# Kernel tuning notes

Measured on AMD Instinct MI355X. Metric: run time of the kernel, lower is better.

Reference implementation:

```python
import jax, jax.numpy as jnp
import numpy as np
from jax import lax


def _maxpool_h(x):
    # MaxPool2d(kernel=(3,1), stride=(2,1), padding=(1,0)) on NCHW.
    # Torch pads with -inf for max pooling.
    return lax.reduce_window(
        x,
        -jnp.inf,
        lax.max,
        window_dimensions=(1, 1, 3, 1),
        window_strides=(1, 1, 2, 1),
        padding=((0, 0), (0, 0), (1, 1), (0, 0)),
    )


def setup_inputs() -> dict:
    key = jax.random.key(0)
    x = jax.random.normal(key, (32, 1, 8192, 256), dtype=jnp.float32)
    return {"x": x}


def reference(x) -> jnp.ndarray:
    out = _maxpool_h(x)  # [B, C, H', W]
    # Per-sample min-max normalization (vectorized over batch instead of the
    # original per-sample python loop).
    mx = jnp.max(out, axis=(1, 2, 3), keepdims=True)
    mn = jnp.min(out, axis=(1, 2, 3), keepdims=True)
    return (out - mn) / (mx - mn)
```

## Files before the change

kernel.cpp:

```cpp
#include <hip/hip_runtime.h>
#include <cfloat>

#define BATCH     32
#define H_IN      8192
#define H_OUT     4096
#define W         256
#define W4        64
#define CH        32
#define BLK_PER_B 32

__device__ __forceinline__ float4 max3_f4(float4 a, float4 b, float4 c) {
    float4 m;
    m.x = fmaxf(a.x, fmaxf(b.x, c.x));
    m.y = fmaxf(a.y, fmaxf(b.y, c.y));
    m.z = fmaxf(a.z, fmaxf(b.z, c.z));
    m.w = fmaxf(a.w, fmaxf(b.w, c.w));
    return m;
}

__global__ __launch_bounds__(256) void pool_partial(
        const float* __restrict__ x, float* __restrict__ out,
        float* __restrict__ partial_min, float* __restrict__ partial_max) {
    const int batch = blockIdx.x >> 5;
    const int blk   = blockIdx.x & 31;
    const int tid   = threadIdx.x;
    const int w4    = tid & 63;
    const int rg    = tid >> 6;
    const int h0    = blk * (BLK_PER_B * 4) + rg * CH;

    const float4* xin = (const float4*)x + (size_t)batch * H_IN * W4 + w4;
    float4*       po  = (float4*)out + ((size_t)batch * H_OUT + h0) * W4 + w4;

    float lmin = FLT_MAX, lmax = -FLT_MAX;

    float4 prev;
    const int r0 = 2 * h0 - 1;
    if (r0 >= 0) prev = xin[(size_t)r0 * W4];
    else         prev = make_float4(-FLT_MAX, -FLT_MAX, -FLT_MAX, -FLT_MAX);

    #pragma unroll 4
    for (int i = 0; i < CH; ++i) {
        const int r = 2 * (h0 + i);
        float4 a = xin[(size_t)r * W4];
        float4 c = xin[(size_t)(r + 1) * W4];
        float4 m = max3_f4(prev, a, c);
        po[(size_t)i * W4] = m;
        prev = c;
        lmax = fmaxf(lmax, fmaxf(fmaxf(m.x, m.y), fmaxf(m.z, m.w)));
        lmin = fminf(lmin, fminf(fminf(m.x, m.y), fminf(m.z, m.w)));
    }

    #pragma unroll
    for (int off = 32; off > 0; off >>= 1) {
        lmax = fmaxf(lmax, __shfl_down(lmax, off, 64));
        lmin = fminf(lmin, __shfl_down(lmin, off, 64));
    }
    __shared__ float smax[4], smin[4];
    const int lane = tid & 63;
    if (lane == 0) { smax[rg] = lmax; smin[rg] = lmin; }
    __syncthreads();
    if (tid == 0) {
        float bmax = smax[0], bmin = smin[0];
        #pragma unroll
        for (int i = 1; i < 4; ++i) {
            bmax = fmaxf(bmax, smax[i]);
            bmin = fminf(bmin, smin[i]);
        }
        partial_max[blockIdx.x] = bmax;
        partial_min[blockIdx.x] = bmin;
    }
}

__global__ void reduce_partials(const float* __restrict__ pmin,
                                const float* __restrict__ pmax,
                                float* __restrict__ stats) {
    const int b = blockIdx.x;
    const int t = threadIdx.x;
    float mn = (t < BLK_PER_B) ? pmin[b * BLK_PER_B + t] : FLT_MAX;
    float mx = (t < BLK_PER_B) ? pmax[b * BLK_PER_B + t] : -FLT_MAX;
    #pragma unroll
    for (int off = 16; off > 0; off >>= 1) {
        mn = fminf(mn, __shfl_down(mn, off, 64));
        mx = fmaxf(mx, __shfl_down(mx, off, 64));
    }
    if (t == 0) {
        stats[2 * b]     = mn;
        stats[2 * b + 1] = 1.0f / (mx - mn);
    }
}

__global__ __launch_bounds__(256) void normalize(float* __restrict__ out,
                                                 const float* __restrict__ stats) {
    const int b   = blockIdx.x >> 8;
    const int blk = blockIdx.x & 255;
    const float mn  = stats[2 * b];
    const float inv = stats[2 * b + 1];
    float4* p = (float4*)out + (size_t)b * (H_OUT * W4);
    const int base = blk * 1024 + threadIdx.x;
    #pragma unroll
    for (int i = 0; i < 4; ++i) {
        const int idx = base + i * 256;
        float4 v = p[idx];
        v.x = (v.x - mn) * inv;
        v.y = (v.y - mn) * inv;
        v.z = (v.z - mn) * inv;
        v.w = (v.w - mn) * inv;
        p[idx] = v;
    }
}

extern "C" void kernel_launch(void* const* d_in, const int* in_sizes, int n_in,
                              void* d_out, int out_size, void* d_ws, size_t ws_size,
                              hipStream_t stream) {
    const float* x   = (const float*)d_in[0];
    float*       out = (float*)d_out;
    float*       ws  = (float*)d_ws;

    float* pmin  = ws;
    float* pmax  = ws + 1024;
    float* stats = ws + 2048;

    pool_partial<<<BATCH * BLK_PER_B, 256, 0, stream>>>(x, out, pmin, pmax);
    reduce_partials<<<BATCH, 64, 0, stream>>>(pmin, pmax, stats);
    normalize<<<BATCH * 256, 256, 0, stream>>>(out, stats);
}
```

Before: 432.6 us.

## Recompute pooling in normalize pass instead of storing and rereading intermediate output

Splits the work into a min/max-only pooling pass that no longer writes the pooled output, and a second pass that recomputes the pooling, reduces the per-batch partials in-block, and writes normalized values directly with nontemporal stores. This removes the intermediate write and the read-modify-write normalize pass, as well as the separate reduce kernel launch. In exchange the input tensor is read twice, so total memory traffic stays roughly similar.

Result: no change. 436.7 us (+0.9%).

```diff
diff --git a/kernel.cpp b/kernel.cpp
--- a/kernel.cpp
+++ b/kernel.cpp
@@ -9,6 +9,8 @@
 #define CH        32
 #define BLK_PER_B 32
 
+typedef float f32x4 __attribute__((ext_vector_type(4)));
+
 __device__ __forceinline__ float4 max3_f4(float4 a, float4 b, float4 c) {
     float4 m;
     m.x = fmaxf(a.x, fmaxf(b.x, c.x));
@@ -18,8 +20,8 @@
     return m;
 }
 
-__global__ __launch_bounds__(256) void pool_partial(
-        const float* __restrict__ x, float* __restrict__ out,
+__global__ __launch_bounds__(256) void pool_minmax(
+        const float* __restrict__ x,
         float* __restrict__ partial_min, float* __restrict__ partial_max) {
     const int batch = blockIdx.x >> 5;
     const int blk   = blockIdx.x & 31;
@@ -29,7 +31,6 @@
     const int h0    = blk * (BLK_PER_B * 4) + rg * CH;
 
     const float4* xin = (const float4*)x + (size_t)batch * H_IN * W4 + w4;
-    float4*       po  = (float4*)out + ((size_t)batch * H_OUT + h0) * W4 + w4;
 
     float lmin = FLT_MAX, lmax = -FLT_MAX;
 
@@ -44,7 +45,6 @@
         float4 a = xin[(size_t)r * W4];
         float4 c = xin[(size_t)(r + 1) * W4];
         float4 m = max3_f4(prev, a, c);
-        po[(size_t)i * W4] = m;
         prev = c;
         lmax = fmaxf(lmax, fmaxf(fmaxf(m.x, m.y), fmaxf(m.z, m.w)));
         lmin = fminf(lmin, fminf(fminf(m.x, m.y), fminf(m.z, m.w)));
@@ -56,8 +56,7 @@
         lmin = fminf(lmin, __shfl_down(lmin, off, 64));
     }
     __shared__ float smax[4], smin[4];
-    const int lane = tid & 63;
-    if (lane == 0) { smax[rg] = lmax; smin[rg] = lmin; }
+    if ((tid & 63) == 0) { smax[rg] = lmax; smin[rg] = lmin; }
     __syncthreads();
     if (tid == 0) {
         float bmax = smax[0], bmin = smin[0];
@@ -71,41 +70,52 @@
     }
 }
 
-__global__ void reduce_partials(const float* __restrict__ pmin,
-                                const float* __restrict__ pmax,
-                                float* __restrict__ stats) {
-    const int b = blockIdx.x;
-    const int t = threadIdx.x;
-    float mn = (t < BLK_PER_B) ? pmin[b * BLK_PER_B + t] : FLT_MAX;
-    float mx = (t < BLK_PER_B) ? pmax[b * BLK_PER_B + t] : -FLT_MAX;
-    #pragma unroll
-    for (int off = 16; off > 0; off >>= 1) {
-        mn = fminf(mn, __shfl_down(mn, off, 64));
-        mx = fmaxf(mx, __shfl_down(mx, off, 64));
+__global__ __launch_bounds__(256) void pool_normalize(
+        const float* __restrict__ x, float* __restrict__ out,
+        const float* __restrict__ pmin, const float* __restrict__ pmax) {
+    const int batch = blockIdx.x >> 5;
+    const int blk   = blockIdx.x & 31;
+    const int tid   = threadIdx.x;
+
+    __shared__ float s_mn, s_inv;
+    if (tid < 64) {
+        float mn = (tid < BLK_PER_B) ? pmin[batch * BLK_PER_B + tid] : FLT_MAX;
+        float mx = (tid < BLK_PER_B) ? pmax[batch * BLK_PER_B + tid] : -FLT_MAX;
+        #pragma unroll
+        for (int off = 16; off > 0; off >>= 1) {
+            mn = fminf(mn, __shfl_down(mn, off, 64));
+            mx = fmaxf(mx, __shfl_down(mx, off, 64));
+        }
+        if (tid == 0) { s_mn = mn; s_inv = 1.0f / (mx - mn); }
     }
-    if (t == 0) {
-        stats[2 * b]     = mn;
-        stats[2 * b + 1] = 1.0f / (mx - mn);
-    }
-}
+    __syncthreads();
+    const float mn  = s_mn;
+    const float inv = s_inv;
 
-__global__ __launch_bounds__(256) void normalize(float* __restrict__ out,
-                                                 const float* __restrict__ stats) {
-    const int b   = blockIdx.x >> 8;
-    const int blk = blockIdx.x & 255;
-    const float mn  = stats[2 * b];
-    const float inv = stats[2 * b + 1];
-    float4* p = (float4*)out + (size_t)b * (H_OUT * W4);
-    const int base = blk * 1024 + threadIdx.x;
-    #pragma unroll
-    for (int i = 0; i < 4; ++i) {
-        const int idx = base + i * 256;
-        float4 v = p[idx];
-        v.x = (v.x - mn) * inv;
-        v.y = (v.y - mn) * inv;
-        v.z = (v.z - mn) * inv;
-        v.w = (v.w - mn) * inv;
-        p[idx] = v;
+    const int w4 = tid & 63;
+    const int rg = tid >> 6;
+    const int h0 = blk * (BLK_PER_B * 4) + rg * CH;
+
+    const float4* xin = (const float4*)x + (size_t)batch * H_IN * W4 + w4;
+    f32x4*        po  = (f32x4*)out + ((size_t)batch * H_OUT + h0) * W4 + w4;
+
+    float4 prev;
+    const int r0 = 2 * h0 - 1;
+    if (r0 >= 0) prev = xin[(size_t)r0 * W4];
+    else         prev = make_float4(-FLT_MAX, -FLT_MAX, -FLT_MAX, -FLT_MAX);
+
+    #pragma unroll 4
+    for (int i = 0; i < CH; ++i) {
+        const int r = 2 * (h0 + i);
+        float4 a = xin[(size_t)r * W4];
+        float4 c = xin[(size_t)(r + 1) * W4];
+        float4 m = max3_f4(prev, a, c);
+        prev = c;
+        f32x4 v = { (m.x - mn) * inv,
+                    (m.y - mn) * inv,
+                    (m.z - mn) * inv,
+                    (m.w - mn) * inv };
+        __builtin_nontemporal_store(v, po + (size_t)i * W4);
     }
 }
 
@@ -116,11 +126,9 @@
     float*       out = (float*)d_out;
     float*       ws  = (float*)d_ws;
 
-    float* pmin  = ws;
-    float* pmax  = ws + 1024;
-    float* stats = ws + 2048;
+    float* pmin = ws;
+    float* pmax = ws + 1024;
 
-    pool_partial<<<BATCH * BLK_PER_B, 256, 0, stream>>>(x, out, pmin, pmax);
-    reduce_partials<<<BATCH, 64, 0, stream>>>(pmin, pmax, stats);
-    normalize<<<BATCH * 256, 256, 0, stream>>>(out, stats);
+    pool_minmax<<<BATCH * BLK_PER_B, 256, 0, stream>>>(x, pmin, pmax);
+    pool_normalize<<<BATCH * BLK_PER_B, 256, 0, stream>>>(x, out, pmin, pmax);
 }
```
